# Kernel optimization log

Measured on AMD Instinct MI355X. Metric: run time of the kernel, lower is better.

## Reference

```python
import jax, jax.numpy as jnp
import numpy as np

H = 4096
W = 4096
C = 3
OUT = 1024
MAX_MIP = 8  # matches init max_mip_level; mip chain is levels 0..MAX_MIP


def setup_inputs() -> dict:
    key = jax.random.key(0)
    k1, k2, k3 = jax.random.split(key, 3)
    data = jax.random.uniform(k1, (1, H, W, C), dtype=jnp.float32)
    texc = jax.random.uniform(k2, (1, OUT, OUT, 2), dtype=jnp.float32)
    # small UV derivatives -> per-pixel texel footprint of a few texels, so the
    # LOD spans several mip levels (exercises cross-level paged gathers)
    texc_deriv = jax.random.normal(k3, (1, OUT, OUT, 4), dtype=jnp.float32) * 2e-3
    return {"data": data, "texc": texc, "texc_deriv": texc_deriv}


def _avg_pool2(x):
    # 2x2 box-filter mipmap reduction, matching virtual_texture_mipmap_fwd
    b, h, w, c = x.shape
    return x.reshape(b, h // 2, 2, w // 2, 2, c).mean(axis=(2, 4))


def _bilinear_wrap(tex, texc):
    # tex: [1,h,w,c]; texc: [1,Ho,Wo,2] in [0,1); boundary_mode='wrap'
    h, w = tex.shape[1], tex.shape[2]
    x = texc[..., 0] * w - 0.5
    y = texc[..., 1] * h - 0.5
    x0f = jnp.floor(x)
    y0f = jnp.floor(y)
    fx = (x - x0f)[..., None]
    fy = (y - y0f)[..., None]
    x0 = x0f.astype(jnp.int32) % w
    y0 = y0f.astype(jnp.int32) % h
    x1 = (x0 + 1) % w
    y1 = (y0 + 1) % h
    t = tex[0]  # [h,w,c]
    top = t[y0, x0] * (1.0 - fx) + t[y0, x1] * fx
    bot = t[y1, x0] * (1.0 - fx) + t[y1, x1] * fx
    return top * (1.0 - fy) + bot * fy  # [1,Ho,Wo,c]


def _forward(data, texc, texc_deriv):
    # LOD from screen-space UV derivatives (nvdiffrast linear-mipmap-linear)
    dudx = texc_deriv[..., 0] * W
    dvdx = texc_deriv[..., 1] * H
    dudy = texc_deriv[..., 2] * W
    dvdy = texc_deriv[..., 3] * H
    rho2 = jnp.maximum(dudx * dudx + dvdx * dvdx, dudy * dudy + dvdy * dvdy)
    lod = 0.5 * jnp.log2(jnp.maximum(rho2, 1e-20))
    lod = jnp.clip(lod, 0.0, float(MAX_MIP))  # [1,Ho,Wo]

    # build mip pyramid (gradients flow back to base texture, matching
    # virtual_texture_mipmap_bwd accumulation)
    mips = [data]
    for _ in range(MAX_MIP):
        mips.append(_avg_pool2(mips[-1]))

    # trilinear: per-level weight w_l = clip(1 - |lod - l|, 0, 1)
    out = jnp.zeros(texc.shape[:-1] + (C,), dtype=data.dtype)
    for lvl in range(MAX_MIP + 1):
        w_l = jnp.clip(1.0 - jnp.abs(lod - float(lvl)), 0.0, 1.0)[..., None]
        out = out + w_l * _bilinear_wrap(mips[lvl], texc)
    return out


def reference(data, texc, texc_deriv):
    return _forward(data, texc, texc_deriv)
```

## Files before the change

kernel.cpp:

```cpp
#include <hip/hip_runtime.h>
#include <hip/hip_bf16.h>


#define TEX_W 4096
#define OUT_N (1024 * 1024)

__global__ void mip_down(const float* __restrict__ in, float* __restrict__ out,
                         int out_size ) {
    int n = out_size * out_size * 3;
    int i = blockIdx.x * blockDim.x + threadIdx.x;
    if (i >= n) return;
    int c = i % 3;
    int p = i / 3;
    int x = p & (out_size - 1);
    int y = p / out_size;
    int in_size = out_size * 2;
    const float* base = in + ((size_t)(2 * y) * in_size + 2 * x) * 3 + c;
    float a = base[0];
    float b = base[3];
    float e = base[(size_t)in_size * 3];
    float d = base[(size_t)in_size * 3 + 3];
    out[i] = (a + b + e + d) * 0.25f;
}

__device__ __forceinline__ const float* mip_base(const float* data, const float* ws, int lvl) {
    if (lvl == 0) return data;
    unsigned off = 16777216u - (16777216u >> (2 * (lvl - 1)));
    return ws + off;
}

__device__ __forceinline__ void sample_level(const float* __restrict__ t, int lvl,
                                             float u, float v, float wgt,
                                             float& r, float& g, float& b) {
    int size = TEX_W >> lvl;
    float fs = (float)size;
    float x = u * fs - 0.5f;
    float y = v * fs - 0.5f;
    float x0f = floorf(x);
    float y0f = floorf(y);
    float fx = x - x0f;
    float fy = y - y0f;
    int m = size - 1;
    int x0 = ((int)x0f) & m;
    int y0 = ((int)y0f) & m;
    int x1 = (x0 + 1) & m;
    int y1 = (y0 + 1) & m;
    const float* p00 = t + ((size_t)y0 * size + x0) * 3;
    const float* p01 = t + ((size_t)y0 * size + x1) * 3;
    const float* p10 = t + ((size_t)y1 * size + x0) * 3;
    const float* p11 = t + ((size_t)y1 * size + x1) * 3;
    float w00 = (1.0f - fx) * (1.0f - fy) * wgt;
    float w01 = fx * (1.0f - fy) * wgt;
    float w10 = (1.0f - fx) * fy * wgt;
    float w11 = fx * fy * wgt;
    r += p00[0] * w00 + p01[0] * w01 + p10[0] * w10 + p11[0] * w11;
    g += p00[1] * w00 + p01[1] * w01 + p10[1] * w10 + p11[1] * w11;
    b += p00[2] * w00 + p01[2] * w01 + p10[2] * w10 + p11[2] * w11;
}

__global__ void vt_sample(const float* __restrict__ data, const float* __restrict__ ws,
                          const float* __restrict__ texc, const float* __restrict__ deriv,
                          float* __restrict__ out) {
    int p = blockIdx.x * blockDim.x + threadIdx.x;
    if (p >= OUT_N) return;

    float2 uv = ((const float2*)texc)[p];
    float4 dv = ((const float4*)deriv)[p];
    float dudx = dv.x * (float)TEX_W;
    float dvdx = dv.y * (float)TEX_W;
    float dudy = dv.z * (float)TEX_W;
    float dvdy = dv.w * (float)TEX_W;
    float rho2 = fmaxf(dudx * dudx + dvdx * dvdx, dudy * dudy + dvdy * dvdy);
    float lod = 0.5f * log2f(fmaxf(rho2, 1e-20f));
    lod = fminf(fmaxf(lod, 0.0f), 8.0f);

    int l0 = (int)floorf(lod);
    if (l0 > 8) l0 = 8;
    float f = lod - (float)l0;
    int l1 = (l0 < 8) ? (l0 + 1) : 8;

    float r = 0.0f, g = 0.0f, b = 0.0f;
    sample_level(mip_base(data, ws, l0), l0, uv.x, uv.y, 1.0f - f, r, g, b);
    sample_level(mip_base(data, ws, l1), l1, uv.x, uv.y, f, r, g, b);

    float* o = out + (size_t)p * 3;
    o[0] = r;
    o[1] = g;
    o[2] = b;
}

extern "C" void kernel_launch(void* const* d_in, const int* in_sizes, int n_in,
                              void* d_out, int out_size, void* d_ws, size_t ws_size,
                              hipStream_t stream) {
    const float* data  = (const float*)d_in[0];
    const float* texc  = (const float*)d_in[1];
    const float* deriv = (const float*)d_in[2];
    float* out = (float*)d_out;
    float* ws  = (float*)d_ws;

    const float* src = data;
    unsigned off = 0;
    int osz = 2048;
    for (int l = 1; l <= 8; ++l) {
        float* dst = ws + off;
        int n = osz * osz * 3;
        int blocks = (n + 255) / 256;
        mip_down<<<blocks, 256, 0, stream>>>(src, dst, osz);
        src = dst;
        off += (unsigned)n;
        osz >>= 1;
    }

    int blocks = (OUT_N + 255) / 256;
    vt_sample<<<blocks, 256, 0, stream>>>(data, ws, texc, deriv, out);
}
```

Baseline: 350.2 us.

## Fuse mip pyramid build into one kernel with fp16 quad-tiled storage

Replaces eight separate mip_down launches with one fused kernel that reads the base texture once and builds levels 1-6 through shared memory, plus a small single-block tail kernel for levels 7-8. Mip levels are stored as fp16 RGB padded to 8 bytes, in 2x2 quad tiles, so each bilinear footprint touches fewer cache lines and less workspace traffic. The sampler reads level 0 in fp32 and the upper levels in fp16. This trades precision on mip levels for bandwidth, and the tail kernel runs on a single block.

After: 338.2 us. -3.4%, faster.

```diff
diff --git a/kernel.cpp b/kernel.cpp
--- a/kernel.cpp
+++ b/kernel.cpp
@@ -1,38 +1,198 @@
 #include <hip/hip_runtime.h>
 #include <hip/hip_bf16.h>
-
-
-#define TEX_W 4096
+#include <hip/hip_fp16.h>
+
+
 #define OUT_N (1024 * 1024)
 
-__global__ void mip_down(const float* __restrict__ in, float* __restrict__ out,
-                         int out_size ) {
-    int n = out_size * out_size * 3;
-    int i = blockIdx.x * blockDim.x + threadIdx.x;
-    if (i >= n) return;
-    int c = i % 3;
-    int p = i / 3;
-    int x = p & (out_size - 1);
-    int y = p / out_size;
-    int in_size = out_size * 2;
-    const float* base = in + ((size_t)(2 * y) * in_size + 2 * x) * 3 + c;
-    float a = base[0];
-    float b = base[3];
-    float e = base[(size_t)in_size * 3];
-    float d = base[(size_t)in_size * 3 + 3];
-    out[i] = (a + b + e + d) * 0.25f;
-}
-
-__device__ __forceinline__ const float* mip_base(const float* data, const float* ws, int lvl) {
-    if (lvl == 0) return data;
-    unsigned off = 16777216u - (16777216u >> (2 * (lvl - 1)));
-    return ws + off;
-}
-
-__device__ __forceinline__ void sample_level(const float* __restrict__ t, int lvl,
-                                             float u, float v, float wgt,
-                                             float& r, float& g, float& b) {
-    int size = TEX_W >> lvl;
+__device__ __forceinline__ unsigned mip_off_b(int lvl) {
+    return (134217728u - (134217728u >> (2 * lvl - 2))) / 3u;
+}
+
+__device__ __forceinline__ uint2 enc3(float r, float g, float b) {
+    __half2 h0 = __floats2half2_rn(r, g);
+    __half2 h1 = __floats2half2_rn(b, 0.0f);
+    uint2 q;
+    q.x = *reinterpret_cast<unsigned*>(&h0);
+    q.y = *reinterpret_cast<unsigned*>(&h1);
+    return q;
+}
+
+__device__ __forceinline__ void dec_acc(uint2 q, float w, float& r, float& g, float& b) {
+    __half2 h0 = *reinterpret_cast<__half2*>(&q.x);
+    __half2 h1 = *reinterpret_cast<__half2*>(&q.y);
+    float2 rg = __half22float2(h0);
+    float2 bb = __half22float2(h1);
+    r = fmaf(rg.x, w, r);
+    g = fmaf(rg.y, w, g);
+    b = fmaf(bb.x, w, b);
+}
+
+__device__ __forceinline__ float3 dec3(uint2 q) {
+    __half2 h0 = *reinterpret_cast<__half2*>(&q.x);
+    __half2 h1 = *reinterpret_cast<__half2*>(&q.y);
+    float2 rg = __half22float2(h0);
+    float2 bb = __half22float2(h1);
+    return float3{rg.x, rg.y, bb.x};
+}
+
+__device__ __forceinline__ float4 avg4(float4 a, float4 b, float4 c, float4 d) {
+    return float4{(a.x + b.x + c.x + d.x) * 0.25f,
+                  (a.y + b.y + c.y + d.y) * 0.25f,
+                  (a.z + b.z + c.z + d.z) * 0.25f, 0.0f};
+}
+
+__device__ __forceinline__ void store_quad(char* p, float4 t00, float4 t01,
+                                           float4 t10, float4 t11) {
+    uint2 e00 = enc3(t00.x, t00.y, t00.z);
+    uint2 e01 = enc3(t01.x, t01.y, t01.z);
+    uint2 e10 = enc3(t10.x, t10.y, t10.z);
+    uint2 e11 = enc3(t11.x, t11.y, t11.z);
+    *(uint4*)p        = make_uint4(e00.x, e00.y, e01.x, e01.y);
+    *(uint4*)(p + 16) = make_uint4(e10.x, e10.y, e11.x, e11.y);
+}
+
+__global__ __launch_bounds__(256) void mip_fused(const float* __restrict__ data,
+                                                 char* __restrict__ wsb) {
+    __shared__ float4 s1[32][33];
+    __shared__ float4 s2[16][17];
+    __shared__ float4 s3[8][9];
+    __shared__ float4 s4[4][5];
+
+    const int t = threadIdx.x;
+    const int bx = blockIdx.x & 63;
+    const int by = blockIdx.x >> 6;
+
+    {
+        int qx = t & 15, qy = t >> 4;
+        int r0 = (by << 6) + (qy << 2);
+        int c0 = (bx << 6) + (qx << 2);
+        const float* p = data + ((size_t)r0 * 4096 + c0) * 3;
+        float4 t00 = {0, 0, 0, 0}, t01 = {0, 0, 0, 0};
+        float4 t10 = {0, 0, 0, 0}, t11 = {0, 0, 0, 0};
+#pragma unroll
+        for (int i = 0; i < 4; ++i) {
+            const float4* rp = (const float4*)(p + (size_t)i * 4096 * 3);
+            float4 A = rp[0], B = rp[1], C = rp[2];
+            float ex = A.x + A.w, ey = A.y + B.x, ez = A.z + B.y;
+            float fx_ = B.z + C.y, fy_ = B.w + C.z, fz_ = C.x + C.w;
+            if (i < 2) {
+                t00.x += ex; t00.y += ey; t00.z += ez;
+                t01.x += fx_; t01.y += fy_; t01.z += fz_;
+            } else {
+                t10.x += ex; t10.y += ey; t10.z += ez;
+                t11.x += fx_; t11.y += fy_; t11.z += fz_;
+            }
+        }
+        t00.x *= 0.25f; t00.y *= 0.25f; t00.z *= 0.25f;
+        t01.x *= 0.25f; t01.y *= 0.25f; t01.z *= 0.25f;
+        t10.x *= 0.25f; t10.y *= 0.25f; t10.z *= 0.25f;
+        t11.x *= 0.25f; t11.y *= 0.25f; t11.z *= 0.25f;
+        s1[2 * qy][2 * qx] = t00;     s1[2 * qy][2 * qx + 1] = t01;
+        s1[2 * qy + 1][2 * qx] = t10; s1[2 * qy + 1][2 * qx + 1] = t11;
+        unsigned gq = (((by << 4) + qy) << 10) + (bx << 4) + qx;
+        store_quad(wsb + ((size_t)gq << 5), t00, t01, t10, t11);
+    }
+    __syncthreads();
+
+    if (t < 64) {
+        int qx = t & 7, qy = t >> 3;
+        int sy = qy << 2, sx = qx << 2;
+        float4 t00 = avg4(s1[sy][sx], s1[sy][sx + 1], s1[sy + 1][sx], s1[sy + 1][sx + 1]);
+        float4 t01 = avg4(s1[sy][sx + 2], s1[sy][sx + 3], s1[sy + 1][sx + 2], s1[sy + 1][sx + 3]);
+        float4 t10 = avg4(s1[sy + 2][sx], s1[sy + 2][sx + 1], s1[sy + 3][sx], s1[sy + 3][sx + 1]);
+        float4 t11 = avg4(s1[sy + 2][sx + 2], s1[sy + 2][sx + 3], s1[sy + 3][sx + 2], s1[sy + 3][sx + 3]);
+        s2[2 * qy][2 * qx] = t00;     s2[2 * qy][2 * qx + 1] = t01;
+        s2[2 * qy + 1][2 * qx] = t10; s2[2 * qy + 1][2 * qx + 1] = t11;
+        unsigned gq = ((by << 3) + qy) * 512 + (bx << 3) + qx;
+        store_quad(wsb + 33554432u + ((size_t)gq << 5), t00, t01, t10, t11);
+    }
+    __syncthreads();
+
+    if (t < 16) {
+        int qx = t & 3, qy = t >> 2;
+        int sy = qy << 2, sx = qx << 2;
+        float4 t00 = avg4(s2[sy][sx], s2[sy][sx + 1], s2[sy + 1][sx], s2[sy + 1][sx + 1]);
+        float4 t01 = avg4(s2[sy][sx + 2], s2[sy][sx + 3], s2[sy + 1][sx + 2], s2[sy + 1][sx + 3]);
+        float4 t10 = avg4(s2[sy + 2][sx], s2[sy + 2][sx + 1], s2[sy + 3][sx], s2[sy + 3][sx + 1]);
+        float4 t11 = avg4(s2[sy + 2][sx + 2], s2[sy + 2][sx + 3], s2[sy + 3][sx + 2], s2[sy + 3][sx + 3]);
+        s3[2 * qy][2 * qx] = t00;     s3[2 * qy][2 * qx + 1] = t01;
+        s3[2 * qy + 1][2 * qx] = t10; s3[2 * qy + 1][2 * qx + 1] = t11;
+        unsigned gq = ((by << 2) + qy) * 256 + (bx << 2) + qx;
+        store_quad(wsb + 41943040u + ((size_t)gq << 5), t00, t01, t10, t11);
+    }
+    __syncthreads();
+
+    if (t < 4) {
+        int qx = t & 1, qy = t >> 1;
+        int sy = qy << 2, sx = qx << 2;
+        float4 t00 = avg4(s3[sy][sx], s3[sy][sx + 1], s3[sy + 1][sx], s3[sy + 1][sx + 1]);
+        float4 t01 = avg4(s3[sy][sx + 2], s3[sy][sx + 3], s3[sy + 1][sx + 2], s3[sy + 1][sx + 3]);
+        float4 t10 = avg4(s3[sy + 2][sx], s3[sy + 2][sx + 1], s3[sy + 3][sx], s3[sy + 3][sx + 1]);
+        float4 t11 = avg4(s3[sy + 2][sx + 2], s3[sy + 2][sx + 3], s3[sy + 3][sx + 2], s3[sy + 3][sx + 3]);
+        s4[2 * qy][2 * qx] = t00;     s4[2 * qy][2 * qx + 1] = t01;
+        s4[2 * qy + 1][2 * qx] = t10; s4[2 * qy + 1][2 * qx + 1] = t11;
+        unsigned gq = ((by << 1) + qy) * 128 + (bx << 1) + qx;
+        store_quad(wsb + 44040192u + ((size_t)gq << 5), t00, t01, t10, t11);
+    }
+    __syncthreads();
+
+    if (t == 0) {
+        float4 t00 = avg4(s4[0][0], s4[0][1], s4[1][0], s4[1][1]);
+        float4 t01 = avg4(s4[0][2], s4[0][3], s4[1][2], s4[1][3]);
+        float4 t10 = avg4(s4[2][0], s4[2][1], s4[3][0], s4[3][1]);
+        float4 t11 = avg4(s4[2][2], s4[2][3], s4[3][2], s4[3][3]);
+        unsigned gq = (unsigned)by * 64u + (unsigned)bx;
+        store_quad(wsb + 44564480u + ((size_t)gq << 5), t00, t01, t10, t11);
+        float4 l6 = avg4(t00, t01, t10, t11);
+        size_t a6 = 44695552u + ((((by >> 1) * 32) + (bx >> 1)) << 5) +
+                    ((by & 1) << 4) + ((bx & 1) << 3);
+        *(uint2*)(wsb + a6) = enc3(l6.x, l6.y, l6.z);
+    }
+}
+
+__global__ __launch_bounds__(256) void mip_tail(char* __restrict__ wsb) {
+    __shared__ float4 s7[32][33];
+    const int t = threadIdx.x;
+
+    {
+        int qx = t & 15, qy = t >> 4;
+        float4 f[4][4];
+#pragma unroll
+        for (int dy = 0; dy < 4; ++dy)
+#pragma unroll
+            for (int dx = 0; dx < 4; ++dx) {
+                int yy = (qy << 2) + dy, xx = (qx << 2) + dx;
+                size_t a = 44695552u + (((yy >> 1) * 32 + (xx >> 1)) << 5) +
+                           ((yy & 1) << 4) + ((xx & 1) << 3);
+                float3 v = dec3(*(const uint2*)(wsb + a));
+                f[dy][dx] = float4{v.x, v.y, v.z, 0.0f};
+            }
+        float4 t00 = avg4(f[0][0], f[0][1], f[1][0], f[1][1]);
+        float4 t01 = avg4(f[0][2], f[0][3], f[1][2], f[1][3]);
+        float4 t10 = avg4(f[2][0], f[2][1], f[3][0], f[3][1]);
+        float4 t11 = avg4(f[2][2], f[2][3], f[3][2], f[3][3]);
+        s7[2 * qy][2 * qx] = t00;     s7[2 * qy][2 * qx + 1] = t01;
+        s7[2 * qy + 1][2 * qx] = t10; s7[2 * qy + 1][2 * qx + 1] = t11;
+        store_quad(wsb + 44728320u + ((size_t)((qy << 4) + qx) << 5), t00, t01, t10, t11);
+    }
+    __syncthreads();
+
+    if (t < 64) {
+        int qx = t & 7, qy = t >> 3;
+        int sy = qy << 2, sx = qx << 2;
+        float4 t00 = avg4(s7[sy][sx], s7[sy][sx + 1], s7[sy + 1][sx], s7[sy + 1][sx + 1]);
+        float4 t01 = avg4(s7[sy][sx + 2], s7[sy][sx + 3], s7[sy + 1][sx + 2], s7[sy + 1][sx + 3]);
+        float4 t10 = avg4(s7[sy + 2][sx], s7[sy + 2][sx + 1], s7[sy + 3][sx], s7[sy + 3][sx + 1]);
+        float4 t11 = avg4(s7[sy + 2][sx + 2], s7[sy + 2][sx + 3], s7[sy + 3][sx + 2], s7[sy + 3][sx + 3]);
+        store_quad(wsb + 44736512u + ((size_t)((qy << 3) + qx) << 5), t00, t01, t10, t11);
+    }
+}
+
+__device__ __forceinline__ void sample_fp16(const char* __restrict__ wsb, int lvl,
+                                            float u, float v, float wgt,
+                                            float& r, float& g, float& b) {
+    int size = 4096 >> lvl;
     float fs = (float)size;
     float x = u * fs - 0.5f;
     float y = v * fs - 0.5f;
@@ -45,10 +205,43 @@
     int y0 = ((int)y0f) & m;
     int x1 = (x0 + 1) & m;
     int y1 = (y0 + 1) & m;
-    const float* p00 = t + ((size_t)y0 * size + x0) * 3;
-    const float* p01 = t + ((size_t)y0 * size + x1) * 3;
-    const float* p10 = t + ((size_t)y1 * size + x0) * 3;
-    const float* p11 = t + ((size_t)y1 * size + x1) * 3;
+    int hs = size >> 1;
+    const char* B = wsb + mip_off_b(lvl);
+    const char* a00 = B + ((((y0 >> 1) * hs) + (x0 >> 1)) << 5) + ((y0 & 1) << 4) + ((x0 & 1) << 3);
+    const char* a01 = B + ((((y0 >> 1) * hs) + (x1 >> 1)) << 5) + ((y0 & 1) << 4) + ((x1 & 1) << 3);
+    const char* a10 = B + ((((y1 >> 1) * hs) + (x0 >> 1)) << 5) + ((y1 & 1) << 4) + ((x0 & 1) << 3);
+    const char* a11 = B + ((((y1 >> 1) * hs) + (x1 >> 1)) << 5) + ((y1 & 1) << 4) + ((x1 & 1) << 3);
+    uint2 q00 = *(const uint2*)a00;
+    uint2 q01 = *(const uint2*)a01;
+    uint2 q10 = *(const uint2*)a10;
+    uint2 q11 = *(const uint2*)a11;
+    float w00 = (1.0f - fx) * (1.0f - fy) * wgt;
+    float w01 = fx * (1.0f - fy) * wgt;
+    float w10 = (1.0f - fx) * fy * wgt;
+    float w11 = fx * fy * wgt;
+    dec_acc(q00, w00, r, g, b);
+    dec_acc(q01, w01, r, g, b);
+    dec_acc(q10, w10, r, g, b);
+    dec_acc(q11, w11, r, g, b);
+}
+
+__device__ __forceinline__ void sample_level0(const float* __restrict__ data,
+                                              float u, float v, float wgt,
+                                              float& r, float& g, float& b) {
+    float x = u * 4096.0f - 0.5f;
+    float y = v * 4096.0f - 0.5f;
+    float x0f = floorf(x);
+    float y0f = floorf(y);
+    float fx = x - x0f;
+    float fy = y - y0f;
+    int x0 = ((int)x0f) & 4095;
+    int y0 = ((int)y0f) & 4095;
+    int x1 = (x0 + 1) & 4095;
+    int y1 = (y0 + 1) & 4095;
+    const float* p00 = data + ((size_t)y0 * 4096 + x0) * 3;
+    const float* p01 = data + ((size_t)y0 * 4096 + x1) * 3;
+    const float* p10 = data + ((size_t)y1 * 4096 + x0) * 3;
+    const float* p11 = data + ((size_t)y1 * 4096 + x1) * 3;
     float w00 = (1.0f - fx) * (1.0f - fy) * wgt;
     float w01 = fx * (1.0f - fy) * wgt;
     float w10 = (1.0f - fx) * fy * wgt;
@@ -58,30 +251,34 @@
     b += p00[2] * w00 + p01[2] * w01 + p10[2] * w10 + p11[2] * w11;
 }
 
-__global__ void vt_sample(const float* __restrict__ data, const float* __restrict__ ws,
-                          const float* __restrict__ texc, const float* __restrict__ deriv,
-                          float* __restrict__ out) {
-    int p = blockIdx.x * blockDim.x + threadIdx.x;
-    if (p >= OUT_N) return;
+__global__ __launch_bounds__(256) void vt_sample(const float* __restrict__ data,
+                                                 const char* __restrict__ wsb,
+                                                 const float* __restrict__ texc,
+                                                 const float* __restrict__ deriv,
+                                                 float* __restrict__ out) {
+    int p = blockIdx.x * 256 + threadIdx.x;
 
     float2 uv = ((const float2*)texc)[p];
     float4 dv = ((const float4*)deriv)[p];
-    float dudx = dv.x * (float)TEX_W;
-    float dvdx = dv.y * (float)TEX_W;
-    float dudy = dv.z * (float)TEX_W;
-    float dvdy = dv.w * (float)TEX_W;
+    float dudx = dv.x * 4096.0f;
+    float dvdx = dv.y * 4096.0f;
+    float dudy = dv.z * 4096.0f;
+    float dvdy = dv.w * 4096.0f;
     float rho2 = fmaxf(dudx * dudx + dvdx * dvdx, dudy * dudy + dvdy * dvdy);
     float lod = 0.5f * log2f(fmaxf(rho2, 1e-20f));
     lod = fminf(fmaxf(lod, 0.0f), 8.0f);
 
-    int l0 = (int)floorf(lod);
-    if (l0 > 8) l0 = 8;
+    int l0 = (int)lod;
     float f = lod - (float)l0;
     int l1 = (l0 < 8) ? (l0 + 1) : 8;
 
     float r = 0.0f, g = 0.0f, b = 0.0f;
-    sample_level(mip_base(data, ws, l0), l0, uv.x, uv.y, 1.0f - f, r, g, b);
-    sample_level(mip_base(data, ws, l1), l1, uv.x, uv.y, f, r, g, b);
+    if (l0 == 0) {
+        sample_level0(data, uv.x, uv.y, 1.0f - f, r, g, b);
+    } else {
+        sample_fp16(wsb, l0, uv.x, uv.y, 1.0f - f, r, g, b);
+    }
+    sample_fp16(wsb, l1, uv.x, uv.y, f, r, g, b);
 
     float* o = out + (size_t)p * 3;
     o[0] = r;
@@ -96,21 +293,9 @@
     const float* texc  = (const float*)d_in[1];
     const float* deriv = (const float*)d_in[2];
     float* out = (float*)d_out;
-    float* ws  = (float*)d_ws;
-
-    const float* src = data;
-    unsigned off = 0;
-    int osz = 2048;
-    for (int l = 1; l <= 8; ++l) {
-        float* dst = ws + off;
-        int n = osz * osz * 3;
-        int blocks = (n + 255) / 256;
-        mip_down<<<blocks, 256, 0, stream>>>(src, dst, osz);
-        src = dst;
-        off += (unsigned)n;
-        osz >>= 1;
-    }
-
-    int blocks = (OUT_N + 255) / 256;
-    vt_sample<<<blocks, 256, 0, stream>>>(data, ws, texc, deriv, out);
-}
+    char* wsb  = (char*)d_ws;
+
+    mip_fused<<<4096, 256, 0, stream>>>(data, wsb);
+    mip_tail<<<1, 256, 0, stream>>>(wsb);
+    vt_sample<<<OUT_N / 256, 256, 0, stream>>>(data, wsb, texc, deriv, out);
+}
```
